# Optimization experiments

Hardware: AMD Instinct MI355X
Metric: run time of the kernel (lower is better)

Reference implementation:

```python
import jax, jax.numpy as jnp
import numpy as np

BS, TPD, D = 16384, 4, 128
G, M = 4, 4096


def setup_inputs() -> dict:
    key = jax.random.key(0)
    k1, k2 = jax.random.split(key)
    return {
        "x": jax.random.normal(k1, (BS, TPD, D), dtype=jnp.float32),
        "embeddings": jax.random.normal(k2, (G, M, D), dtype=jnp.float32),
        "count": jnp.zeros((G, M), dtype=jnp.float32),
    }


def reference(x, embeddings, count):
    bs, tpd, d = x.shape
    g, m, _ = embeddings.shape
    # (BS, TPD, D) -> (N, G, D) -> (G, N, D), N = BS*TPD/G
    xg = x.reshape(-1, g, d).transpose(1, 0, 2)
    # squared euclidean distances (argmin identical to cdist argmin)
    x2 = jnp.sum(xg * xg, axis=-1)[:, :, None]            # (G, N, 1)
    e2 = jnp.sum(embeddings * embeddings, axis=-1)[:, None, :]  # (G, 1, M)
    dist = x2 + e2 - 2.0 * jnp.einsum('gnd,gmd->gnm', xg, embeddings)  # (G, N, M)
    indices = jnp.argmin(dist, axis=-1)                   # (G, N) int
    # usage-count scatter add (buffer update in torch forward)
    new_count = count.at[jnp.arange(g)[:, None], indices].add(1.0)
    # gather quantized embeddings: (G, N, D)
    x_quant = embeddings[jnp.arange(g)[:, None], indices]
    x_quant = x_quant.transpose(1, 0, 2).reshape(bs, tpd, d)
    ind_out = indices.transpose(1, 0).reshape(bs, tpd)
    return (x_quant, ind_out, new_count)
```

## Files before the change

kernel.cpp:

```cpp
#include <hip/hip_runtime.h>

#define G 4
#define M 4096
#define D 128
#define NQ 16384
#define NROWS 65536
#define OFF_IND 8388608
#define OFF_CNT (OFF_IND + NROWS)
#define DELTA 0.02f

typedef unsigned int u32;
typedef unsigned short u16;
typedef __attribute__((ext_vector_type(8))) short bf16x8;
typedef __attribute__((ext_vector_type(4))) float f32x4;
typedef __attribute__((ext_vector_type(16))) float f32x16;

__device__ __forceinline__ u16 f2bf(float f) {
    u32 u = __float_as_uint(f);
    return (u16)((u + 0x7FFFu + ((u >> 16) & 1u)) >> 16);
}
__device__ __forceinline__ float bf2f(u16 b) { return __uint_as_float((u32)b << 16); }

union bfpack { bf16x8 v; u32 u[4]; };

__device__ __forceinline__ void gload16(const void* gsrc, void* ldsdst) {
    __builtin_amdgcn_global_load_lds(
        (const __attribute__((address_space(1))) u32*)gsrc,
        (__attribute__((address_space(3))) u32*)ldsdst,
        16, 0, 0);
}


__global__ __launch_bounds__(256) void prep_all(const float* __restrict__ emb,
                                                u32* __restrict__ efrag,
                                                float* __restrict__ e2f,
                                                int* __restrict__ flagcnt) {
    __shared__ float part[4][32];
    const int tid = threadIdx.x, w = tid >> 6;
    const int g = blockIdx.x >> 7, mt = blockIdx.x & 127;
    u32* chunk = efrag + (size_t)(g * 128 + mt) * 4096;
    float ss = 0.f;
#pragma unroll
    for (int rep = 0; rep < 2; ++rep) {
        const int idx = rep * 256 + tid;
        const int kk = idx >> 6, lane = idx & 63;
        const int m = mt * 32 + (lane & 31);
        const int k = kk * 16 + (lane >> 5) * 8;
        const float* src = emb + ((size_t)g * M + m) * D + k;
        const float4 a = *(const float4*)src;
        const float4 b = *(const float4*)(src + 4);
        const float v[8] = {a.x, a.y, a.z, a.w, b.x, b.y, b.z, b.w};
#pragma unroll
        for (int i = 0; i < 8; ++i) ss = fmaf(v[i], v[i], ss);
        u32 hi[4], lo[4];
#pragma unroll
        for (int i = 0; i < 4; ++i) {
            const float v0 = v[2 * i], v1 = v[2 * i + 1];
            const u16 h0 = f2bf(v0), h1 = f2bf(v1);
            const u16 l0 = f2bf(v0 - bf2f(h0)), l1 = f2bf(v1 - bf2f(h1));
            hi[i] = (u32)h0 | ((u32)h1 << 16);
            lo[i] = (u32)l0 | ((u32)l1 << 16);
        }
        *(uint4*)(chunk + (size_t)((kk * 2 + 0) * 64 + lane) * 4) = make_uint4(hi[0], hi[1], hi[2], hi[3]);
        *(uint4*)(chunk + (size_t)((kk * 2 + 1) * 64 + lane) * 4) = make_uint4(lo[0], lo[1], lo[2], lo[3]);
    }
    ss += __shfl_xor(ss, 32, 64);
    if ((tid & 63) < 32) part[w][tid & 31] = ss;
    __syncthreads();
    if (tid < 32)
        e2f[(size_t)g * M + mt * 32 + tid] = part[0][tid] + part[1][tid] + part[2][tid] + part[3][tid];
    if (blockIdx.x == 0 && tid == 0) *flagcnt = 0;
}

__global__ __launch_bounds__(256, 3) void vq_mfma4(const float* __restrict__ x,
                                                   const u32* __restrict__ efrag,
                                                   const float* __restrict__ e2f,
                                                   float* __restrict__ out) {
    __shared__ float e2s[2048];
    __shared__ u32 ebuf[2][4096];

    const int tid = threadIdx.x, w = tid >> 6, lane = tid & 63;
    const int combo = blockIdx.x & 7;
    const int g = combo >> 1, half = combo & 1;
    const int qb = blockIdx.x >> 3;

    const float* e2g = e2f + (size_t)g * M + half * 2048;
    for (int i = tid; i < 512; i += 256) ((float4*)e2s)[i] = ((const float4*)e2g)[i];

    const int qrow = qb * 128 + w * 32 + (lane & 31);
    bf16x8 xh[8], xl[8];
#pragma unroll
    for (int kk = 0; kk < 8; ++kk) {
        const int k = kk * 16 + (lane >> 5) * 8;
        const float* src = x + ((size_t)qrow * 4 + g) * D + k;
        const float4 a = *(const float4*)src;
        const float4 b = *(const float4*)(src + 4);
        const float v[8] = {a.x, a.y, a.z, a.w, b.x, b.y, b.z, b.w};
        bfpack ph, pl;
#pragma unroll
        for (int i = 0; i < 4; ++i) {
            const float v0 = -2.0f * v[2 * i], v1 = -2.0f * v[2 * i + 1];
            const u16 h0 = f2bf(v0), h1 = f2bf(v1);
            const u16 l0 = f2bf(v0 - bf2f(h0)), l1 = f2bf(v1 - bf2f(h1));
            ph.u[i] = (u32)h0 | ((u32)h1 << 16);
            pl.u[i] = (u32)l0 | ((u32)l1 << 16);
        }
        xh[kk] = ph.v;
        xl[kk] = pl.v;
    }

    float b1[16], b2[16];
    int i1[16];
#pragma unroll
    for (int r = 0; r < 16; ++r) { b1[r] = 3.4e38f; b2[r] = 3.4e38f; i1[r] = 0; }

    const char* eg = (const char*)(efrag + (size_t)(g * 128 + half * 64) * 4096);
#pragma unroll
    for (int j = 0; j < 4; ++j)
        gload16(eg + j * 4096 + w * 1024 + lane * 16,
                (char*)ebuf[0] + j * 4096 + w * 1024);
    __syncthreads();

    int cur = 0;
    for (int t = 0; t < 64; ++t) {
        if (t < 63) {
            const char* src = eg + (size_t)(t + 1) * 16384;
#pragma unroll
            for (int j = 0; j < 4; ++j)
                gload16(src + j * 4096 + w * 1024 + lane * 16,
                        (char*)ebuf[cur ^ 1] + j * 4096 + w * 1024);
        }
        const bf16x8* bp = (const bf16x8*)ebuf[cur];
        const float e2c = e2s[t * 32 + (lane & 31)];
        f32x16 acc;
#pragma unroll
        for (int r = 0; r < 16; ++r) acc[r] = e2c;
#pragma unroll
        for (int kk = 0; kk < 8; ++kk) {
            const bf16x8 bh = bp[(kk * 2 + 0) * 64 + lane];
            const bf16x8 bl = bp[(kk * 2 + 1) * 64 + lane];
            acc = __builtin_amdgcn_mfma_f32_32x32x16_bf16(xl[kk], bh, acc, 0, 0, 0);
            acc = __builtin_amdgcn_mfma_f32_32x32x16_bf16(xh[kk], bl, acc, 0, 0, 0);
            acc = __builtin_amdgcn_mfma_f32_32x32x16_bf16(xh[kk], bh, acc, 0, 0, 0);
        }
        const int mcol = half * 2048 + t * 32 + (lane & 31);
#pragma unroll
        for (int r = 0; r < 16; ++r) {
            const float s = acc[r];
            b2[r] = __builtin_amdgcn_fmed3f(s, b1[r], b2[r]);
            i1[r] = (s < b1[r]) ? mcol : i1[r];
            b1[r] = fminf(b1[r], s);
        }
        __syncthreads();
        cur ^= 1;
    }

#pragma unroll
    for (int r = 0; r < 16; ++r) {
        float v1 = b1[r], v2 = b2[r];
        int j1 = i1[r];
#pragma unroll
        for (int off = 1; off < 32; off <<= 1) {
            const float o1 = __shfl_xor(v1, off, 64);
            const int   oj = __shfl_xor(j1, off, 64);
            const float o2 = __shfl_xor(v2, off, 64);
            v2 = fminf(fminf(v2, o2), fmaxf(v1, o1));
            if (o1 < v1 || (o1 == v1 && oj < j1)) { v1 = o1; j1 = oj; }
        }
        if ((lane & 31) == 0) {
            const int q = qb * 128 + w * 32 + (r & 3) + 8 * (r >> 2) + 4 * (lane >> 5);
            float* rowbase = out + (size_t)(q * 4 + g) * D;
            *(float4*)(rowbase + half * 4) =
                make_float4(v1, v2, __int_as_float(j1), 0.f);
        }
    }
}

__global__ __launch_bounds__(256) void gather_merge(const float* __restrict__ emb,
                                                    float* __restrict__ out,
                                                    int* __restrict__ flagcnt,
                                                    int* __restrict__ flaglist) {
    __shared__ int sm[64];
    const int tid = threadIdx.x;
    const int qid0 = blockIdx.x * 64;
    const int g = qid0 >> 14;
    if (tid < 64) {
        const int qid = qid0 + tid;
        const int n = qid & 16383;
        float* rowbase = out + (size_t)(n * 4 + g) * D;
        const float4 p0 = *(const float4*)(rowbase);
        const float4 p1 = *(const float4*)(rowbase + 4);
        const float v1a = p0.x, v2a = p0.y;
        const float v1b = p1.x, v2b = p1.y;
        const int ia = __float_as_int(p0.z), ib = __float_as_int(p1.z);
        const float v1 = fminf(v1a, v1b);
        const int i = (v1b < v1a) ? ib : ia;
        const float v2 = fminf(fminf(v2a, v2b), fmaxf(v1a, v1b));
        out[(size_t)OFF_IND + (size_t)n * 4 + g] = (float)i;
        if (v2 - v1 > DELTA) {
            atomicAdd(out + OFF_CNT + (size_t)g * M + i, 1.0f);
        } else {
            const int pos = atomicAdd(flagcnt, 1);
            flaglist[pos] = qid;
        }
        sm[tid] = i;
    }
    __syncthreads();
#pragma unroll
    for (int p = 0; p < 8; ++p) {
        const int t2 = p * 8 + (tid >> 5);
        const int lane = tid & 31;
        const int n = (qid0 + t2) & 16383;
        const int m = sm[t2];
        const float4 v = ((const float4*)(emb + ((size_t)g * M + m) * D))[lane];
        ((float4*)(out + (size_t)(n * 4 + g) * D))[lane] = v;
    }
}

__global__ __launch_bounds__(256) void recheck2(const float* __restrict__ x,
                                                const float* __restrict__ emb,
                                                const int* __restrict__ flagcnt,
                                                const int* __restrict__ flaglist,
                                                float* __restrict__ out) {
    __shared__ float xs[D];
    __shared__ double wv[4];
    __shared__ int wi[4];
    __shared__ int sbj;
    const int tid = threadIdx.x;
    int nf = *flagcnt;
    if (nf > NROWS) nf = NROWS;
    for (int it = blockIdx.x; it < nf; it += gridDim.x) {
        const int qid = flaglist[it];
        const int g = qid >> 14, n = qid & 16383;
        __syncthreads();
        if (tid < 32) ((float4*)xs)[tid] = ((const float4*)(x + ((size_t)n * 4 + g) * D))[tid];
        __syncthreads();
        double best = 1e300;
        int bi = 0;
        for (int j = 0; j < 16; ++j) {
            const int m = tid + j * 256;
            const float* e = emb + ((size_t)g * M + m) * D;
            double dot = 0.0, ee = 0.0;
            for (int k = 0; k < D; k += 4) {
                const float4 ev = *(const float4*)(e + k);
                const double e0 = ev.x, e1 = ev.y, e2v = ev.z, e3 = ev.w;
                dot = fma((double)xs[k + 0], e0, dot);
                dot = fma((double)xs[k + 1], e1, dot);
                dot = fma((double)xs[k + 2], e2v, dot);
                dot = fma((double)xs[k + 3], e3, dot);
                ee = fma(e0, e0, ee); ee = fma(e1, e1, ee);
                ee = fma(e2v, e2v, ee); ee = fma(e3, e3, ee);
            }
            const double s = ee - 2.0 * dot;
            if (s < best) { best = s; bi = m; }
        }
        for (int off = 1; off < 64; off <<= 1) {
            const double ob = __shfl_xor(best, off, 64);
            const int oi = __shfl_xor(bi, off, 64);
            if (ob < best || (ob == best && oi < bi)) { best = ob; bi = oi; }
        }
        if ((tid & 63) == 0) { wv[tid >> 6] = best; wi[tid >> 6] = bi; }
        __syncthreads();
        if (tid == 0) {
            double bv = wv[0];
            int bj = wi[0];
            for (int u = 1; u < 4; ++u)
                if (wv[u] < bv || (wv[u] == bv && wi[u] < bj)) { bv = wv[u]; bj = wi[u]; }
            out[(size_t)OFF_IND + (size_t)n * 4 + g] = (float)bj;
            atomicAdd(out + OFF_CNT + (size_t)g * M + bj, 1.0f);
            sbj = bj;
        }
        __syncthreads();
        if (tid < 32) {
            const int bj = sbj;
            ((float4*)(out + (size_t)(n * 4 + g) * D))[tid] =
                ((const float4*)(emb + ((size_t)g * M + bj) * D))[tid];
        }
    }
}


#define QT 64
#define MT 128
#define KT 32
#define XPAD 132
#define EPAD 36

__global__ __launch_bounds__(256) void e2d_kernel(const float* __restrict__ emb,
                                                  double* __restrict__ e2) {
    int row = blockIdx.x * 4 + (threadIdx.x >> 6);
    int lane = threadIdx.x & 63;
    const float2 v = ((const float2*)(emb + (size_t)row * D))[lane];
    double s = (double)v.x * (double)v.x + (double)v.y * (double)v.y;
#pragma unroll
    for (int off = 1; off < 64; off <<= 1) s += __shfl_xor(s, off, 64);
    if (lane == 0) e2[row] = s;
}

__global__ __launch_bounds__(256) void argmin_kernel(const float* __restrict__ x,
                                                     const float* __restrict__ emb,
                                                     const double* __restrict__ e2,
                                                     float* __restrict__ out) {
    __shared__ float xs[QT][XPAD];
    __shared__ float es[MT][EPAD];
    const int g = blockIdx.x >> 8;
    const int n0 = (blockIdx.x & 255) * QT;
    const int tid = threadIdx.x;
    const int tm = tid & 15;
    const int tq = tid >> 4;
#pragma unroll
    for (int it = 0; it < 8; ++it) {
        int idx = it * 256 + tid;
        int r = idx >> 5, c2 = idx & 31;
        const float4 v = ((const float4*)(x + ((size_t)((n0 + r) * 4 + g)) * D))[c2];
        *(float4*)&xs[r][c2 * 4] = v;
    }
    double best[4];
    int bm[4];
#pragma unroll
    for (int qi = 0; qi < 4; ++qi) { best[qi] = 1e300; bm[qi] = 0; }
    const double* e2g = e2 + (size_t)g * M;
    const float* eg = emb + (size_t)g * M * D;
    for (int mc = 0; mc < M / MT; ++mc) {
        const int m0 = mc * MT;
        double acc[4][8];
#pragma unroll
        for (int qi = 0; qi < 4; ++qi)
#pragma unroll
            for (int mi = 0; mi < 8; ++mi) acc[qi][mi] = 0.0;
        for (int kc = 0; kc < D / KT; ++kc) {
            __syncthreads();
#pragma unroll
            for (int it = 0; it < 4; ++it) {
                int idx = it * 256 + tid;
                int r = idx >> 3, c2 = idx & 7;
                const float4 v = ((const float4*)(eg + (size_t)(m0 + r) * D + kc * KT))[c2];
                *(float4*)&es[r][c2 * 4] = v;
            }
            __syncthreads();
#pragma unroll
            for (int kk = 0; kk < KT; kk += 4) {
                double xv[4][4];
#pragma unroll
                for (int qi = 0; qi < 4; ++qi) {
                    const float4 v = *(const float4*)&xs[tq + 16 * qi][kc * KT + kk];
                    xv[qi][0] = v.x; xv[qi][1] = v.y; xv[qi][2] = v.z; xv[qi][3] = v.w;
                }
#pragma unroll
                for (int mi = 0; mi < 8; ++mi) {
                    const float4 v = *(const float4*)&es[tm + 16 * mi][kk];
                    const double e0 = v.x, e1 = v.y, e2v = v.z, e3 = v.w;
#pragma unroll
                    for (int qi = 0; qi < 4; ++qi) {
                        acc[qi][mi] = fma(xv[qi][0], e0, acc[qi][mi]);
                        acc[qi][mi] = fma(xv[qi][1], e1, acc[qi][mi]);
                        acc[qi][mi] = fma(xv[qi][2], e2v, acc[qi][mi]);
                        acc[qi][mi] = fma(xv[qi][3], e3, acc[qi][mi]);
                    }
                }
            }
        }
#pragma unroll
        for (int mi = 0; mi < 8; ++mi) {
            const int m = m0 + tm + 16 * mi;
            const double e2m = e2g[m];
#pragma unroll
            for (int qi = 0; qi < 4; ++qi) {
                const double s = e2m - 2.0 * acc[qi][mi];
                if (s < best[qi]) { best[qi] = s; bm[qi] = m; }
            }
        }
    }
#pragma unroll
    for (int qi = 0; qi < 4; ++qi) {
        double v = best[qi];
        int i = bm[qi];
#pragma unroll
        for (int off = 1; off < 16; off <<= 1) {
            const double ov = __shfl_xor(v, off, 64);
            const int oi = __shfl_xor(i, off, 64);
            if (ov < v || (ov == v && oi < i)) { v = ov; i = oi; }
        }
        if (tm == 0) {
            const int n = n0 + tq + 16 * qi;
            out[(size_t)OFF_IND + (size_t)n * 4 + g] = (float)i;
            atomicAdd(out + OFF_CNT + (size_t)g * M + i, 1.0f);
        }
    }
}

__global__ __launch_bounds__(256) void gather_kernel(const float* __restrict__ emb,
                                                     const float* __restrict__ indf,
                                                     float* __restrict__ xq) {
    const int rid = blockIdx.x * 8 + (threadIdx.x >> 5);
    const int lane = threadIdx.x & 31;
    const int g = rid & 3;
    const int m = (int)indf[rid];
    const float4 v = ((const float4*)(emb + ((size_t)g * M + m) * D))[lane];
    ((float4*)(xq + (size_t)rid * D))[lane] = v;
}


extern "C" void kernel_launch(void* const* d_in, const int* in_sizes, int n_in,
                              void* d_out, int out_size, void* d_ws, size_t ws_size,
                              hipStream_t stream) {
    const float* x   = (const float*)d_in[0];
    const float* emb = (const float*)d_in[1];
    const float* cnt = (const float*)d_in[2];
    float* out = (float*)d_out;

    if (ws_size >= 8716544) {
        u32*   efrag    = (u32*)d_ws;
        float* e2fp     = (float*)((char*)d_ws + 8388608);
        int*   flagcnt  = (int*)((char*)d_ws + 8454144);
        int*   flaglist = (int*)((char*)d_ws + 8454400);

        hipLaunchKernelGGL(prep_all, dim3(512), dim3(256), 0, stream,
                           emb, efrag, e2fp, flagcnt);
        hipMemcpyAsync(out + OFF_CNT, cnt, (size_t)G * M * sizeof(float),
                       hipMemcpyDeviceToDevice, stream);
        hipLaunchKernelGGL(vq_mfma4, dim3(1024), dim3(256), 0, stream,
                           x, efrag, e2fp, out);
        hipLaunchKernelGGL(gather_merge, dim3(1024), dim3(256), 0, stream,
                           emb, out, flagcnt, flaglist);
        hipLaunchKernelGGL(recheck2, dim3(2048), dim3(256), 0, stream,
                           x, emb, flagcnt, flaglist, out);
    } else {
        double* e2 = (double*)d_ws;
        hipLaunchKernelGGL(e2d_kernel, dim3(4096), dim3(256), 0, stream, emb, e2);
        hipMemcpyAsync(out + OFF_CNT, cnt, (size_t)G * M * sizeof(float),
                       hipMemcpyDeviceToDevice, stream);
        hipLaunchKernelGGL(argmin_kernel, dim3((NQ / QT) * G), dim3(256), 0, stream,
                           x, emb, e2, out);
        hipLaunchKernelGGL(gather_kernel, dim3(NROWS / 8), dim3(256), 0, stream,
                           emb, out + OFF_IND, out);
    }
}
```

Baseline: 366.3 us.

## Replace split-bf16 three-MFMA distance with single fp16 MFMA and widen recheck margin

The distance GEMM drops the hi/lo bf16 split (three MFMAs per k-step) and uses a single fp16 MFMA per k-step on fp16-converted x and embeddings. This cuts MFMA work by about two thirds and halves the embedding fragment buffer and its LDS footprint. To make up for the lower precision, the near-tie recheck margin DELTA grows from 0.02 to 0.08, so more rows may be flagged for exact recheck. The change also raises the occupancy hint to 4 blocks, rotates each block's starting codebook tile to spread load traffic, and folds the count copy into the prep kernel so the separate memcpy goes away.

Measured after the change: 434.5 us. 18.6% more time.

```diff
diff --git a/kernel.cpp b/kernel.cpp
--- a/kernel.cpp
+++ b/kernel.cpp
@@ -7,21 +7,15 @@
 #define NROWS 65536
 #define OFF_IND 8388608
 #define OFF_CNT (OFF_IND + NROWS)
-#define DELTA 0.02f
+#define DELTA 0.08f
 
 typedef unsigned int u32;
 typedef unsigned short u16;
-typedef __attribute__((ext_vector_type(8))) short bf16x8;
+typedef __attribute__((ext_vector_type(8))) _Float16 f16x8;
 typedef __attribute__((ext_vector_type(4))) float f32x4;
 typedef __attribute__((ext_vector_type(16))) float f32x16;
 
-__device__ __forceinline__ u16 f2bf(float f) {
-    u32 u = __float_as_uint(f);
-    return (u16)((u + 0x7FFFu + ((u >> 16) & 1u)) >> 16);
-}
-__device__ __forceinline__ float bf2f(u16 b) { return __uint_as_float((u32)b << 16); }
-
-union bfpack { bf16x8 v; u32 u[4]; };
+union hpack { f16x8 v; u32 u[4]; _Float16 h[8]; };
 
 __device__ __forceinline__ void gload16(const void* gsrc, void* ldsdst) {
     __builtin_amdgcn_global_load_lds(
@@ -32,13 +26,15 @@
 
 
 __global__ __launch_bounds__(256) void prep_all(const float* __restrict__ emb,
+                                                const float* __restrict__ cnt,
                                                 u32* __restrict__ efrag,
                                                 float* __restrict__ e2f,
+                                                float* __restrict__ outcnt,
                                                 int* __restrict__ flagcnt) {
     __shared__ float part[4][32];
     const int tid = threadIdx.x, w = tid >> 6;
     const int g = blockIdx.x >> 7, mt = blockIdx.x & 127;
-    u32* chunk = efrag + (size_t)(g * 128 + mt) * 4096;
+    u32* chunk = efrag + (size_t)(g * 128 + mt) * 2048;
     float ss = 0.f;
 #pragma unroll
     for (int rep = 0; rep < 2; ++rep) {
@@ -50,45 +46,44 @@
         const float4 a = *(const float4*)src;
         const float4 b = *(const float4*)(src + 4);
         const float v[8] = {a.x, a.y, a.z, a.w, b.x, b.y, b.z, b.w};
-#pragma unroll
-        for (int i = 0; i < 8; ++i) ss = fmaf(v[i], v[i], ss);
-        u32 hi[4], lo[4];
-#pragma unroll
-        for (int i = 0; i < 4; ++i) {
-            const float v0 = v[2 * i], v1 = v[2 * i + 1];
-            const u16 h0 = f2bf(v0), h1 = f2bf(v1);
-            const u16 l0 = f2bf(v0 - bf2f(h0)), l1 = f2bf(v1 - bf2f(h1));
-            hi[i] = (u32)h0 | ((u32)h1 << 16);
-            lo[i] = (u32)l0 | ((u32)l1 << 16);
-        }
-        *(uint4*)(chunk + (size_t)((kk * 2 + 0) * 64 + lane) * 4) = make_uint4(hi[0], hi[1], hi[2], hi[3]);
-        *(uint4*)(chunk + (size_t)((kk * 2 + 1) * 64 + lane) * 4) = make_uint4(lo[0], lo[1], lo[2], lo[3]);
+        hpack p;
+#pragma unroll
+        for (int i = 0; i < 8; ++i) {
+            ss = fmaf(v[i], v[i], ss);
+            p.h[i] = (_Float16)v[i];
+        }
+        *(uint4*)(chunk + (size_t)(kk * 64 + lane) * 4) =
+            make_uint4(p.u[0], p.u[1], p.u[2], p.u[3]);
     }
     ss += __shfl_xor(ss, 32, 64);
     if ((tid & 63) < 32) part[w][tid & 31] = ss;
     __syncthreads();
     if (tid < 32)
-        e2f[(size_t)g * M + mt * 32 + tid] = part[0][tid] + part[1][tid] + part[2][tid] + part[3][tid];
+        e2f[(size_t)g * M + mt * 32 + tid] =
+            part[0][tid] + part[1][tid] + part[2][tid] + part[3][tid];
+    else if (tid >= 64 && tid < 96)
+        outcnt[(size_t)g * M + mt * 32 + (tid - 64)] = cnt[(size_t)g * M + mt * 32 + (tid - 64)];
     if (blockIdx.x == 0 && tid == 0) *flagcnt = 0;
 }
 
-__global__ __launch_bounds__(256, 3) void vq_mfma4(const float* __restrict__ x,
+__global__ __launch_bounds__(256, 4) void vq_mfma5(const float* __restrict__ x,
                                                    const u32* __restrict__ efrag,
                                                    const float* __restrict__ e2f,
                                                    float* __restrict__ out) {
     __shared__ float e2s[2048];
-    __shared__ u32 ebuf[2][4096];
+    __shared__ u32 ebuf[2][2048];
 
     const int tid = threadIdx.x, w = tid >> 6, lane = tid & 63;
     const int combo = blockIdx.x & 7;
     const int g = combo >> 1, half = combo & 1;
     const int qb = blockIdx.x >> 3;
+    const int rot = (qb * 23) & 63;
 
     const float* e2g = e2f + (size_t)g * M + half * 2048;
     for (int i = tid; i < 512; i += 256) ((float4*)e2s)[i] = ((const float4*)e2g)[i];
 
     const int qrow = qb * 128 + w * 32 + (lane & 31);
-    bf16x8 xh[8], xl[8];
+    f16x8 xh[8];
 #pragma unroll
     for (int kk = 0; kk < 8; ++kk) {
         const int k = kk * 16 + (lane >> 5) * 8;
@@ -96,17 +91,10 @@
         const float4 a = *(const float4*)src;
         const float4 b = *(const float4*)(src + 4);
         const float v[8] = {a.x, a.y, a.z, a.w, b.x, b.y, b.z, b.w};
-        bfpack ph, pl;
-#pragma unroll
-        for (int i = 0; i < 4; ++i) {
-            const float v0 = -2.0f * v[2 * i], v1 = -2.0f * v[2 * i + 1];
-            const u16 h0 = f2bf(v0), h1 = f2bf(v1);
-            const u16 l0 = f2bf(v0 - bf2f(h0)), l1 = f2bf(v1 - bf2f(h1));
-            ph.u[i] = (u32)h0 | ((u32)h1 << 16);
-            pl.u[i] = (u32)l0 | ((u32)l1 << 16);
-        }
-        xh[kk] = ph.v;
-        xl[kk] = pl.v;
+        hpack p;
+#pragma unroll
+        for (int i = 0; i < 8; ++i) p.h[i] = (_Float16)(-2.0f * v[i]);
+        xh[kk] = p.v;
     }
 
     float b1[16], b2[16];
@@ -114,36 +102,33 @@
 #pragma unroll
     for (int r = 0; r < 16; ++r) { b1[r] = 3.4e38f; b2[r] = 3.4e38f; i1[r] = 0; }
 
-    const char* eg = (const char*)(efrag + (size_t)(g * 128 + half * 64) * 4096);
-#pragma unroll
-    for (int j = 0; j < 4; ++j)
-        gload16(eg + j * 4096 + w * 1024 + lane * 16,
-                (char*)ebuf[0] + j * 4096 + w * 1024);
+    const char* eg = (const char*)(efrag + (size_t)(g * 128 + half * 64) * 2048);
+#pragma unroll
+    for (int j = 0; j < 2; ++j)
+        gload16(eg + (size_t)rot * 8192 + w * 2048 + j * 1024 + lane * 16,
+                (char*)ebuf[0] + w * 2048 + j * 1024);
     __syncthreads();
 
-    int cur = 0;
     for (int t = 0; t < 64; ++t) {
+        const int cur = t & 1;
+        const int cidx = (t + rot) & 63;
         if (t < 63) {
-            const char* src = eg + (size_t)(t + 1) * 16384;
-#pragma unroll
-            for (int j = 0; j < 4; ++j)
-                gload16(src + j * 4096 + w * 1024 + lane * 16,
-                        (char*)ebuf[cur ^ 1] + j * 4096 + w * 1024);
-        }
-        const bf16x8* bp = (const bf16x8*)ebuf[cur];
-        const float e2c = e2s[t * 32 + (lane & 31)];
+            const char* src = eg + (size_t)(((t + 1 + rot) & 63)) * 8192;
+#pragma unroll
+            for (int j = 0; j < 2; ++j)
+                gload16(src + w * 2048 + j * 1024 + lane * 16,
+                        (char*)ebuf[cur ^ 1] + w * 2048 + j * 1024);
+        }
+        const f16x8* bp = (const f16x8*)ebuf[cur];
+        const float e2c = e2s[cidx * 32 + (lane & 31)];
         f32x16 acc;
 #pragma unroll
         for (int r = 0; r < 16; ++r) acc[r] = e2c;
 #pragma unroll
-        for (int kk = 0; kk < 8; ++kk) {
-            const bf16x8 bh = bp[(kk * 2 + 0) * 64 + lane];
-            const bf16x8 bl = bp[(kk * 2 + 1) * 64 + lane];
-            acc = __builtin_amdgcn_mfma_f32_32x32x16_bf16(xl[kk], bh, acc, 0, 0, 0);
-            acc = __builtin_amdgcn_mfma_f32_32x32x16_bf16(xh[kk], bl, acc, 0, 0, 0);
-            acc = __builtin_amdgcn_mfma_f32_32x32x16_bf16(xh[kk], bh, acc, 0, 0, 0);
-        }
-        const int mcol = half * 2048 + t * 32 + (lane & 31);
+        for (int kk = 0; kk < 8; ++kk)
+            acc = __builtin_amdgcn_mfma_f32_32x32x16_f16(xh[kk], bp[kk * 64 + lane],
+                                                         acc, 0, 0, 0);
+        const int mcol = half * 2048 + cidx * 32 + (lane & 31);
 #pragma unroll
         for (int r = 0; r < 16; ++r) {
             const float s = acc[r];
@@ -152,7 +137,6 @@
             b1[r] = fminf(b1[r], s);
         }
         __syncthreads();
-        cur ^= 1;
     }
 
 #pragma unroll
@@ -409,17 +393,15 @@
     const float* cnt = (const float*)d_in[2];
     float* out = (float*)d_out;
 
-    if (ws_size >= 8716544) {
+    if (ws_size >= 4522240) {
         u32*   efrag    = (u32*)d_ws;
-        float* e2fp     = (float*)((char*)d_ws + 8388608);
-        int*   flagcnt  = (int*)((char*)d_ws + 8454144);
-        int*   flaglist = (int*)((char*)d_ws + 8454400);
+        float* e2fp     = (float*)((char*)d_ws + 4194304);
+        int*   flagcnt  = (int*)((char*)d_ws + 4259840);
+        int*   flaglist = (int*)((char*)d_ws + 4260096);
 
         hipLaunchKernelGGL(prep_all, dim3(512), dim3(256), 0, stream,
-                           emb, efrag, e2fp, flagcnt);
-        hipMemcpyAsync(out + OFF_CNT, cnt, (size_t)G * M * sizeof(float),
-                       hipMemcpyDeviceToDevice, stream);
-        hipLaunchKernelGGL(vq_mfma4, dim3(1024), dim3(256), 0, stream,
+                           emb, cnt, efrag, e2fp, out + OFF_CNT, flagcnt);
+        hipLaunchKernelGGL(vq_mfma5, dim3(1024), dim3(256), 0, stream,
                            x, efrag, e2fp, out);
         hipLaunchKernelGGL(gather_merge, dim3(1024), dim3(256), 0, stream,
                            emb, out, flagcnt, flaglist);
```
